# Performance work log

Measured on AMD Instinct MI355X. Metric: run time of the kernel, lower is better.

## Reference

```python
import jax, jax.numpy as jnp
import numpy as np

LX, LY = 256, 256
K_CLASSES = 4
N_SWEEPS = 2
N_SITES = LX * LY

# 8-neighborhood offsets (Moore neighborhood), border handled by clipping
_OFFSETS = np.array([[-1, -1], [-1, 0], [-1, 1],
                     [0, -1],           [0, 1],
                     [1, -1],  [1, 0],  [1, 1]], dtype=np.int32)


def setup_inputs() -> dict:
    key = jax.random.key(0)
    k1, k2, k3, k4 = jax.random.split(key, 4)
    X_init = jax.random.randint(k1, (LX, LY), 0, K_CLASSES).astype(jnp.int32)
    perm = jax.random.permutation(k2, jnp.arange(N_SITES)).astype(jnp.int32)
    uniforms = jax.random.uniform(k3, (N_SWEEPS, N_SITES), dtype=jnp.float32)
    beta = jax.random.uniform(k4, (), dtype=jnp.float32) + 0.5  # Potts coupling
    return {"X_init": X_init, "perm": perm, "uniforms": uniforms,
            "beta": beta, "K": K_CLASSES}


def reference(X_init, perm, uniforms, beta, K):
    lx, ly = X_init.shape
    off = jnp.asarray(_OFFSETS)              # (8, 2)
    classes = jnp.arange(K)                  # (K,)

    def update_one_site(X, uv, r):
        u, v = jnp.unravel_index(uv, (lx, ly))
        uu = jnp.clip(u + off[:, 0], 0, lx - 1)   # (8,) neighbor rows
        vv = jnp.clip(v + off[:, 1], 0, ly - 1)   # (8,) neighbor cols
        neigh = X[uu, vv]                          # (8,) dynamic gather
        # Potts potential: p_k proportional to exp(beta * #{neighbors == k})
        counts = (neigh[None, :] == classes[:, None]).sum(axis=1)  # (K,)
        probs = jax.nn.softmax(beta * counts.astype(jnp.float32))  # (K,) sums to 1
        # inverse-CDF categorical sample, as in the original cumsum < r
        x_sample = jnp.count_nonzero(jnp.cumsum(probs) < r)
        return X.at[u, v].set(x_sample.astype(X.dtype))  # scatter write

    def one_sweep(X, rs):
        def body(Xc, inp):
            uv, r = inp
            return update_one_site(Xc, uv, r), None
        X, _ = jax.lax.scan(body, X, (perm, rs))
        return X, None

    X_final, _ = jax.lax.scan(one_sweep, X_init, uniforms)  # N_SWEEPS sweeps
    return X_final
```

## Files before the change

kernel.cpp:

```cpp
#include <hip/hip_runtime.h>
#include <math.h>

#define NSITES 65536
#define WIN 4096
#define NW 16
#define RMAX 64


__device__ __forceinline__ int agg_pos(int v, int* c, int vmax) {
  int pos = 0;
  const int lane = threadIdx.x & 63;
  for (int vv = 1; vv <= vmax; ++vv) {
    unsigned long long m = __ballot(v == vv);
    if (m) {
      int leader = __ffsll((long long)m) - 1;
      int base = 0;
      if (lane == leader) base = atomicAdd(&c[vv], (int)__popcll(m));
      base = __shfl(base, leader);
      if (v == vv) pos = base + (int)__popcll(m & ((1ull << lane) - 1ull));
    }
  }
  return pos;
}

__global__ __launch_bounds__(1024) void GibbsSched_kernel(
    const int* __restrict__ perm, const float* __restrict__ uni,
    uint2* __restrict__ recpk, int* __restrict__ ends) {
  __shared__ unsigned short posg[NSITES];
  __shared__ unsigned short lvl[WIN];
  __shared__ int cnt[RMAX + 1], coff[RMAX + 1];
  __shared__ int chg, bmax;
  const int tid = threadIdx.x;
  const int w = blockIdx.x;
  const int wbase = w * WIN;

  for (int g = tid; g < NSITES / 8; g += 1024)
    ((uint4*)posg)[g] = make_uint4(0u, 0u, 0u, 0u);
  for (int i = tid; i <= RMAX; i += 1024) { cnt[i] = 0; coff[i] = 0; }
  if (tid == 0) bmax = 0;
  __syncthreads();

  int uvk[4];
#pragma unroll
  for (int k = 0; k < 4; ++k) {
    const int lt = tid + k * 1024;
    uvk[k] = perm[wbase + lt];
    posg[uvk[k]] = (unsigned short)(lt + 1);
  }
  __syncthreads();

  unsigned short pred[4][8];
  int myl[4];
#pragma unroll
  for (int k = 0; k < 4; ++k) {
    const int lt = tid + k * 1024;
    const int uv = uvk[k], u = uv >> 8, v = uv & 255;
    const int um = u ? u - 1 : 0, up = u < 255 ? u + 1 : 255;
    const int vm = v ? v - 1 : 0, vp = v < 255 ? v + 1 : 255;
    const int nb8[8] = {(um << 8) | vm, (um << 8) | v, (um << 8) | vp,
                        (u << 8) | vm,                 (u << 8) | vp,
                        (up << 8) | vm, (up << 8) | v, (up << 8) | vp};
#pragma unroll
    for (int j = 0; j < 8; ++j) {
      const int p = posg[nb8[j]];
      pred[k][j] = (p && p - 1 < lt) ? (unsigned short)(p - 1)
                                     : (unsigned short)0xFFFF;
    }
    lvl[lt] = 1;
    myl[k] = 1;
  }
  __syncthreads();

  for (int pass = 0; pass < 128; ++pass) {
    if (tid == 0) chg = 0;
    __syncthreads();
    bool ch = false;
#pragma unroll
    for (int k = 0; k < 4; ++k) {
      int m = 0;
#pragma unroll
      for (int j = 0; j < 8; ++j) {
        const unsigned short p = pred[k][j];
        if (p != 0xFFFF) m = max(m, (int)lvl[p]);
      }
      const int nl = m + 1;
      if (nl != myl[k]) {
        myl[k] = nl;
        lvl[tid + k * 1024] = (unsigned short)nl;
        ch = true;
      }
    }
    if (ch) chg = 1;
    __syncthreads();
    if (chg == 0) break;
  }

#pragma unroll
  for (int k = 0; k < 4; ++k) atomicMax(&bmax, myl[k]);
  __syncthreads();
  const int vmax = bmax;

#pragma unroll
  for (int k = 0; k < 4; ++k) (void)agg_pos(myl[k], cnt, vmax);
  __syncthreads();
  if (tid == 0) {
    int e = 0;
    for (int r = 0; r < RMAX; ++r) {
      coff[r] = e;
      e += cnt[r];
      ends[w * RMAX + r] = e;
    }
  }
  __syncthreads();

#pragma unroll
  for (int k = 0; k < 4; ++k) {
    const int pos = agg_pos(myl[k], coff, vmax);
    const int lt = tid + k * 1024;
    const int gp = wbase + pos;
    recpk[gp] = make_uint2((unsigned)uvk[k],
                           __float_as_uint(uni[wbase + lt]));
    recpk[NSITES + gp] = make_uint2((unsigned)uvk[k],
                                    __float_as_uint(uni[NSITES + wbase + lt]));
  }
}

__device__ __forceinline__ void do_update(unsigned char* cell,
                                          const unsigned int* cellw,
                                          const float4* ctab, unsigned uvv,
                                          float r) {
  const int u = uvv >> 8, v = (int)(uvv & 255u);
  const int um = u ? u - 1 : 0, up = u < 255 ? u + 1 : 255;
  const int vm = v ? v - 1 : 0, vp = v < 255 ? v + 1 : 255;
  const int cb = vm >> 2;
  const int sh0 = (vm & 3) << 3;
  const int shv = (v - vm) << 3;
  const int shp = (vp - vm) << 3;
  int acc = 0;
  {
    const unsigned int* rw = cellw + (um << 6) + cb;
    const unsigned long long wd =
        ((unsigned long long)rw[1] << 32) | (unsigned long long)rw[0];
    const unsigned wl = (unsigned)(wd >> sh0);
    acc += 1 << ((wl & 255u) << 2);
    acc += 1 << (((wl >> shv) & 255u) << 2);
    acc += 1 << (((wl >> shp) & 255u) << 2);
  }
  {
    const unsigned int* rw = cellw + (u << 6) + cb;
    const unsigned long long wd =
        ((unsigned long long)rw[1] << 32) | (unsigned long long)rw[0];
    const unsigned wl = (unsigned)(wd >> sh0);
    acc += 1 << ((wl & 255u) << 2);
    acc += 1 << (((wl >> shp) & 255u) << 2);
  }
  {
    const unsigned int* rw = cellw + (up << 6) + cb;
    const unsigned long long wd =
        ((unsigned long long)rw[1] << 32) | (unsigned long long)rw[0];
    const unsigned wl = (unsigned)(wd >> sh0);
    acc += 1 << ((wl & 255u) << 2);
    acc += 1 << (((wl >> shv) & 255u) << 2);
    acc += 1 << (((wl >> shp) & 255u) << 2);
  }
  const int n0 = acc & 15, n1 = (acc >> 4) & 15, n2 = (acc >> 8) & 15;
  const float4 c = ctab[n0 + 9 * n1 + 81 * n2];
  int cnt = (c.x < r) ? 1 : 0;
  cnt += (c.y < r) ? 1 : 0;
  cnt += (c.z < r) ? 1 : 0;
  cnt += (c.w < r) ? 1 : 0;
  cell[uvv] = (unsigned char)cnt;
}

__device__ __forceinline__ void run_rounds(unsigned char* cell,
                                           const unsigned int* cellw,
                                           const float4* ctab, const int* le,
                                           const uint2 (&R)[4], int tid) {
  int b = 0, e = le[1];
  for (int rd = 1; rd < RMAX; ++rd) {
    if (b >= WIN) break;
    const int nb = e;
    const int ne = (rd + 1 < RMAX) ? le[rd + 1] : e;
#pragma unroll
    for (int k = 0; k < 4; ++k) {
      const int s = tid + (k << 10);
      if (s >= b && s < e)
        do_update(cell, cellw, ctab, R[k].x, __uint_as_float(R[k].y));
    }
    __syncthreads();
    b = nb;
    e = ne;
  }
}

__global__ __launch_bounds__(1024) void GibbsSampler_90443421319469_kernel(
    const int* __restrict__ Xi, const uint2* __restrict__ recpk,
    const float* __restrict__ betap, const int* __restrict__ ends,
    int* __restrict__ out) {
#pragma clang fp contract(off)
  __shared__ __align__(16) unsigned int cellw[NSITES / 4];
  __shared__ float4 ctab[732];
  __shared__ int lend[NW * RMAX];
  unsigned char* cell = (unsigned char*)cellw;
  const int tid = threadIdx.x;
  const float beta = betap[0];

  uint2 ra[4], rb[4];
#pragma unroll
  for (int k = 0; k < 4; ++k) ra[k] = recpk[tid + (k << 10)];

  for (int g = tid; g < NSITES / 4; g += 1024) {
    int4 x = ((const int4*)Xi)[g];
    cellw[g] = (unsigned)(x.x & 255) | ((unsigned)(x.y & 255) << 8) |
               ((unsigned)(x.z & 255) << 16) | ((unsigned)(x.w & 255) << 24);
  }
  lend[tid] = ends[tid];
  for (int t = tid; t < 729; t += 1024) {
    const int n0 = t % 9, n1 = (t / 9) % 9, n2 = t / 81;
    const int n3 = 8 - n0 - n1 - n2;
    float4 val = make_float4(2.f, 2.f, 2.f, 2.f);
    if (n3 >= 0) {
      const int mx = max(max(n0, n1), max(n2, n3));
      const float xm = beta * (float)mx;
      const float x0 = beta * (float)n0;
      const float x1 = beta * (float)n1;
      const float x2 = beta * (float)n2;
      const float x3 = beta * (float)n3;
      const float e0 = (float)exp((double)(x0 - xm));
      const float e1 = (float)exp((double)(x1 - xm));
      const float e2 = (float)exp((double)(x2 - xm));
      const float e3 = (float)exp((double)(x3 - xm));
      const float s = ((e0 + e1) + e2) + e3;
      const float c0 = e0 / s;
      const float c1 = c0 + e1 / s;
      const float c2 = c1 + e2 / s;
      const float c3 = c2 + e3 / s;
      val = make_float4(c0, c1, c2, c3);
    }
    ctab[t] = val;
  }
  __syncthreads();

  for (int w = 0; w < 2 * NW; ++w) {
    const int ww = w & (NW - 1);
    const int* le = &lend[ww * RMAX];
    const int wn = w + 1;
    const uint2* rpn = recpk + (wn >> 4) * NSITES + (wn & (NW - 1)) * WIN;
    if ((w & 1) == 0) {
      if (wn < 2 * NW) {
#pragma unroll
        for (int k = 0; k < 4; ++k) rb[k] = rpn[tid + (k << 10)];
      }
      run_rounds(cell, cellw, ctab, le, ra, tid);
    } else {
      if (wn < 2 * NW) {
#pragma unroll
        for (int k = 0; k < 4; ++k) ra[k] = rpn[tid + (k << 10)];
      }
      run_rounds(cell, cellw, ctab, le, rb, tid);
    }
  }

  for (int g = tid; g < NSITES / 4; g += 1024) {
    const unsigned p = cellw[g];
    int4 o;
    o.x = (int)(p & 255u);
    o.y = (int)((p >> 8) & 255u);
    o.z = (int)((p >> 16) & 255u);
    o.w = (int)((p >> 24) & 255u);
    ((int4*)out)[g] = o;
  }
}

extern "C" void kernel_launch(void* const* d_in, const int* in_sizes, int n_in,
                              void* d_out, int out_size, void* d_ws,
                              size_t ws_size, hipStream_t stream) {
  const int* Xi = (const int*)d_in[0];
  const int* perm = (const int*)d_in[1];
  const float* uni = (const float*)d_in[2];
  const float* beta = (const float*)d_in[3];
  int* out = (int*)d_out;

  char* ws = (char*)d_ws;
  uint2* recpk = (uint2*)ws;
  int* ends = (int*)(ws + 2 * NSITES * 8);

  GibbsSched_kernel<<<dim3(NW), dim3(1024), 0, stream>>>(perm, uni, recpk,
                                                         ends);
  GibbsSampler_90443421319469_kernel<<<dim3(1), dim3(1024), 0, stream>>>(
      Xi, recpk, beta, ends, out);
}
```

Baseline: 213.8 us.

## Finish small tail rounds in a single wavefront without block barriers

When a round holds 64 or fewer updates, the remaining rounds of the window are handed to wave 0. It reads its records straight from global memory, prefetching the next round, and runs through them without block-wide __syncthreads, so the long tail of small dependency rounds stops paying one full-block barrier each. The round bounds are made wave-uniform with readfirstlane, and a uniform fast path skips per-thread range checks when a round covers a full 1024 chunk. The risk is that larger later rounds get serialized onto one wave, and that correctness now depends on wavefront lockstep ordering between dependent rounds, with no LDS fence between them.

```diff
diff --git a/kernel.cpp b/kernel.cpp
--- a/kernel.cpp
+++ b/kernel.cpp
@@ -175,17 +175,56 @@
 __device__ __forceinline__ void run_rounds(unsigned char* cell,
                                            const unsigned int* cellw,
                                            const float4* ctab, const int* le,
-                                           const uint2 (&R)[4], int tid) {
-  int b = 0, e = le[1];
+                                           const uint2 (&R)[4], int tid,
+                                           const uint2* __restrict__ rp) {
+  const int wave = tid >> 6, lane = tid & 63;
+  int b = 0;
+  int e = __builtin_amdgcn_readfirstlane(le[1]);
   for (int rd = 1; rd < RMAX; ++rd) {
     if (b >= WIN) break;
+    if (e - b <= 64) {
+      if (wave == 0) {
+        int tb = b, te = e, trd = rd;
+        uint2 cur = make_uint2(0u, 0u);
+        if (tb + lane < te) cur = rp[tb + lane];
+        while (tb < WIN) {
+          const int tnb = te;
+          const int tne = (trd + 1 < RMAX)
+                              ? __builtin_amdgcn_readfirstlane(le[trd + 1])
+                              : te;
+          uint2 nxt = make_uint2(0u, 0u);
+          if (tnb + lane < tne) nxt = rp[tnb + lane];
+          if (tb + lane < te)
+            do_update(cell, cellw, ctab, cur.x, __uint_as_float(cur.y));
+          for (int s = tb + lane + 64; s < te; s += 64) {
+            const uint2 rc = rp[s];
+            do_update(cell, cellw, ctab, rc.x, __uint_as_float(rc.y));
+          }
+          cur = nxt;
+          tb = tnb;
+          te = tne;
+          ++trd;
+        }
+      }
+      __syncthreads();
+      return;
+    }
     const int nb = e;
-    const int ne = (rd + 1 < RMAX) ? le[rd + 1] : e;
+    const int ne = (rd + 1 < RMAX)
+                       ? __builtin_amdgcn_readfirstlane(le[rd + 1])
+                       : e;
 #pragma unroll
     for (int k = 0; k < 4; ++k) {
-      const int s = tid + (k << 10);
-      if (s >= b && s < e)
-        do_update(cell, cellw, ctab, R[k].x, __uint_as_float(R[k].y));
+      const int kb = k << 10;
+      if (e > kb && b < kb + 1024) {
+        if (b <= kb && kb + 1024 <= e) {
+          do_update(cell, cellw, ctab, R[k].x, __uint_as_float(R[k].y));
+        } else {
+          const int s = tid + kb;
+          if (s >= b && s < e)
+            do_update(cell, cellw, ctab, R[k].x, __uint_as_float(R[k].y));
+        }
+      }
     }
     __syncthreads();
     b = nb;
@@ -244,6 +283,7 @@
   for (int w = 0; w < 2 * NW; ++w) {
     const int ww = w & (NW - 1);
     const int* le = &lend[ww * RMAX];
+    const uint2* rpc = recpk + (w >> 4) * NSITES + ww * WIN;
     const int wn = w + 1;
     const uint2* rpn = recpk + (wn >> 4) * NSITES + (wn & (NW - 1)) * WIN;
     if ((w & 1) == 0) {
@@ -251,13 +291,13 @@
 #pragma unroll
         for (int k = 0; k < 4; ++k) rb[k] = rpn[tid + (k << 10)];
       }
-      run_rounds(cell, cellw, ctab, le, ra, tid);
+      run_rounds(cell, cellw, ctab, le, ra, tid, rpc);
     } else {
       if (wn < 2 * NW) {
 #pragma unroll
         for (int k = 0; k < 4; ++k) ra[k] = rpn[tid + (k << 10)];
       }
-      run_rounds(cell, cellw, ctab, le, rb, tid);
+      run_rounds(cell, cellw, ctab, le, rb, tid, rpc);
     }
   }
 
```

New measurement: 230.2 us. 1.08x slower.

## Fuse scheduling and sampling kernels with a global atomic flag handoff

Applied to the files above, without the earlier changes.

Merges the level-scheduling kernel and the single-block sampler into one launch of NW blocks. Blocks 1..15 build their window schedules and signal through a global atomic counter, while block 0 builds its own, spins until the rest finish, then runs the sequential sampling phase. This removes one kernel launch and the gap between the two kernels, but adds a hipMemsetAsync and a spin-wait that relies on all blocks being co-resident. It also halves RMAX to 32, which shrinks the round tables but would give wrong results if any window needs more than 31 dependency levels.

```diff
diff --git a/kernel.cpp b/kernel.cpp
--- a/kernel.cpp
+++ b/kernel.cpp
@@ -4,7 +4,7 @@
 #define NSITES 65536
 #define WIN 4096
 #define NW 16
-#define RMAX 64
+#define RMAX 32
 
 
 __device__ __forceinline__ int agg_pos(int v, int* c, int vmax) {
@@ -21,108 +21,6 @@
     }
   }
   return pos;
-}
-
-__global__ __launch_bounds__(1024) void GibbsSched_kernel(
-    const int* __restrict__ perm, const float* __restrict__ uni,
-    uint2* __restrict__ recpk, int* __restrict__ ends) {
-  __shared__ unsigned short posg[NSITES];
-  __shared__ unsigned short lvl[WIN];
-  __shared__ int cnt[RMAX + 1], coff[RMAX + 1];
-  __shared__ int chg, bmax;
-  const int tid = threadIdx.x;
-  const int w = blockIdx.x;
-  const int wbase = w * WIN;
-
-  for (int g = tid; g < NSITES / 8; g += 1024)
-    ((uint4*)posg)[g] = make_uint4(0u, 0u, 0u, 0u);
-  for (int i = tid; i <= RMAX; i += 1024) { cnt[i] = 0; coff[i] = 0; }
-  if (tid == 0) bmax = 0;
-  __syncthreads();
-
-  int uvk[4];
-#pragma unroll
-  for (int k = 0; k < 4; ++k) {
-    const int lt = tid + k * 1024;
-    uvk[k] = perm[wbase + lt];
-    posg[uvk[k]] = (unsigned short)(lt + 1);
-  }
-  __syncthreads();
-
-  unsigned short pred[4][8];
-  int myl[4];
-#pragma unroll
-  for (int k = 0; k < 4; ++k) {
-    const int lt = tid + k * 1024;
-    const int uv = uvk[k], u = uv >> 8, v = uv & 255;
-    const int um = u ? u - 1 : 0, up = u < 255 ? u + 1 : 255;
-    const int vm = v ? v - 1 : 0, vp = v < 255 ? v + 1 : 255;
-    const int nb8[8] = {(um << 8) | vm, (um << 8) | v, (um << 8) | vp,
-                        (u << 8) | vm,                 (u << 8) | vp,
-                        (up << 8) | vm, (up << 8) | v, (up << 8) | vp};
-#pragma unroll
-    for (int j = 0; j < 8; ++j) {
-      const int p = posg[nb8[j]];
-      pred[k][j] = (p && p - 1 < lt) ? (unsigned short)(p - 1)
-                                     : (unsigned short)0xFFFF;
-    }
-    lvl[lt] = 1;
-    myl[k] = 1;
-  }
-  __syncthreads();
-
-  for (int pass = 0; pass < 128; ++pass) {
-    if (tid == 0) chg = 0;
-    __syncthreads();
-    bool ch = false;
-#pragma unroll
-    for (int k = 0; k < 4; ++k) {
-      int m = 0;
-#pragma unroll
-      for (int j = 0; j < 8; ++j) {
-        const unsigned short p = pred[k][j];
-        if (p != 0xFFFF) m = max(m, (int)lvl[p]);
-      }
-      const int nl = m + 1;
-      if (nl != myl[k]) {
-        myl[k] = nl;
-        lvl[tid + k * 1024] = (unsigned short)nl;
-        ch = true;
-      }
-    }
-    if (ch) chg = 1;
-    __syncthreads();
-    if (chg == 0) break;
-  }
-
-#pragma unroll
-  for (int k = 0; k < 4; ++k) atomicMax(&bmax, myl[k]);
-  __syncthreads();
-  const int vmax = bmax;
-
-#pragma unroll
-  for (int k = 0; k < 4; ++k) (void)agg_pos(myl[k], cnt, vmax);
-  __syncthreads();
-  if (tid == 0) {
-    int e = 0;
-    for (int r = 0; r < RMAX; ++r) {
-      coff[r] = e;
-      e += cnt[r];
-      ends[w * RMAX + r] = e;
-    }
-  }
-  __syncthreads();
-
-#pragma unroll
-  for (int k = 0; k < 4; ++k) {
-    const int pos = agg_pos(myl[k], coff, vmax);
-    const int lt = tid + k * 1024;
-    const int gp = wbase + pos;
-    recpk[gp] = make_uint2((unsigned)uvk[k],
-                           __float_as_uint(uni[wbase + lt]));
-    recpk[NSITES + gp] = make_uint2((unsigned)uvk[k],
-                                    __float_as_uint(uni[NSITES + wbase + lt]));
-  }
 }
 
 __device__ __forceinline__ void do_update(unsigned char* cell,
@@ -194,15 +92,134 @@
 }
 
 __global__ __launch_bounds__(1024) void GibbsSampler_90443421319469_kernel(
-    const int* __restrict__ Xi, const uint2* __restrict__ recpk,
-    const float* __restrict__ betap, const int* __restrict__ ends,
-    int* __restrict__ out) {
+    const int* __restrict__ Xi, const int* __restrict__ perm,
+    const float* __restrict__ uni, const float* __restrict__ betap,
+    uint2* __restrict__ recpk, int* __restrict__ ends,
+    int* __restrict__ flag, int* __restrict__ out) {
 #pragma clang fp contract(off)
-  __shared__ __align__(16) unsigned int cellw[NSITES / 4];
-  __shared__ float4 ctab[732];
-  __shared__ int lend[NW * RMAX];
+  __shared__ __align__(16) unsigned char smem[139552];
+  unsigned short* posg = (unsigned short*)smem;
+  unsigned short* lvl = (unsigned short*)(smem + 131072);
+  int* cnt = (int*)(smem + 139264);
+  int* coff = (int*)(smem + 139396);
+  int* chg = (int*)(smem + 139528);
+  int* bmax = (int*)(smem + 139532);
+  unsigned int* cellw = (unsigned int*)smem;
+  float4* ctab = (float4*)(smem + 65536);
+  int* lend = (int*)(smem + 77248);
+
+  const int tid = threadIdx.x;
+  const int w = blockIdx.x;
+  const int wbase = w * WIN;
+
+  for (int g = tid; g < NSITES / 8; g += 1024)
+    ((uint4*)posg)[g] = make_uint4(0u, 0u, 0u, 0u);
+  for (int i = tid; i <= RMAX; i += 1024) { cnt[i] = 0; coff[i] = 0; }
+  if (tid == 0) *bmax = 0;
+  __syncthreads();
+
+  int uvk[4];
+#pragma unroll
+  for (int k = 0; k < 4; ++k) {
+    const int lt = tid + k * 1024;
+    uvk[k] = perm[wbase + lt];
+    posg[uvk[k]] = (unsigned short)(lt + 1);
+  }
+  __syncthreads();
+
+  unsigned short pred[4][8];
+  int myl[4];
+#pragma unroll
+  for (int k = 0; k < 4; ++k) {
+    const int lt = tid + k * 1024;
+    const int uv = uvk[k], u = uv >> 8, v = uv & 255;
+    const int um = u ? u - 1 : 0, up = u < 255 ? u + 1 : 255;
+    const int vm = v ? v - 1 : 0, vp = v < 255 ? v + 1 : 255;
+    const int nb8[8] = {(um << 8) | vm, (um << 8) | v, (um << 8) | vp,
+                        (u << 8) | vm,                 (u << 8) | vp,
+                        (up << 8) | vm, (up << 8) | v, (up << 8) | vp};
+#pragma unroll
+    for (int j = 0; j < 8; ++j) {
+      const int p = posg[nb8[j]];
+      pred[k][j] = (p && p - 1 < lt) ? (unsigned short)(p - 1)
+                                     : (unsigned short)0xFFFF;
+    }
+    lvl[lt] = 1;
+    myl[k] = 1;
+  }
+  __syncthreads();
+
+  for (int pass = 0; pass < 128; ++pass) {
+    if (tid == 0) *chg = 0;
+    __syncthreads();
+    bool ch = false;
+#pragma unroll
+    for (int k = 0; k < 4; ++k) {
+      int m = 0;
+#pragma unroll
+      for (int j = 0; j < 8; ++j) {
+        const unsigned short p = pred[k][j];
+        if (p != 0xFFFF) m = max(m, (int)lvl[p]);
+      }
+      const int nl = m + 1;
+      if (nl != myl[k]) {
+        myl[k] = nl;
+        lvl[tid + k * 1024] = (unsigned short)nl;
+        ch = true;
+      }
+    }
+    if (ch) *chg = 1;
+    __syncthreads();
+    if (*chg == 0) break;
+  }
+
+#pragma unroll
+  for (int k = 0; k < 4; ++k) atomicMax(bmax, myl[k]);
+  __syncthreads();
+  const int vmax = *bmax;
+
+#pragma unroll
+  for (int k = 0; k < 4; ++k) (void)agg_pos(myl[k], cnt, vmax);
+  __syncthreads();
+  if (tid == 0) {
+    int e = 0;
+    for (int r = 0; r < RMAX; ++r) {
+      coff[r] = e;
+      e += cnt[r];
+      ends[w * RMAX + r] = e;
+    }
+  }
+  __syncthreads();
+
+#pragma unroll
+  for (int k = 0; k < 4; ++k) {
+    const int pos = agg_pos(myl[k], coff, vmax);
+    const int lt = tid + k * 1024;
+    const int gp = wbase + pos;
+    recpk[gp] = make_uint2((unsigned)uvk[k],
+                           __float_as_uint(uni[wbase + lt]));
+    recpk[NSITES + gp] = make_uint2((unsigned)uvk[k],
+                                    __float_as_uint(uni[NSITES + wbase + lt]));
+  }
+  __syncthreads();
+
+  if (w != 0) {
+    if (tid == 0) {
+      __threadfence();
+      atomicAdd(flag, 1);
+    }
+    return;
+  }
+
+  if (tid == 0) {
+    while (__hip_atomic_load(flag, __ATOMIC_RELAXED,
+                             __HIP_MEMORY_SCOPE_AGENT) < NW - 1)
+      __builtin_amdgcn_s_sleep(2);
+    __threadfence();
+  }
+  __syncthreads();
+
   unsigned char* cell = (unsigned char*)cellw;
-  const int tid = threadIdx.x;
   const float beta = betap[0];
 
   uint2 ra[4], rb[4];
@@ -214,7 +231,7 @@
     cellw[g] = (unsigned)(x.x & 255) | ((unsigned)(x.y & 255) << 8) |
                ((unsigned)(x.z & 255) << 16) | ((unsigned)(x.w & 255) << 24);
   }
-  lend[tid] = ends[tid];
+  if (tid < NW * RMAX) lend[tid] = ends[tid];
   for (int t = tid; t < 729; t += 1024) {
     const int n0 = t % 9, n1 = (t / 9) % 9, n2 = t / 81;
     const int n3 = 8 - n0 - n1 - n2;
@@ -241,12 +258,12 @@
   }
   __syncthreads();
 
-  for (int w = 0; w < 2 * NW; ++w) {
-    const int ww = w & (NW - 1);
+  for (int ww2 = 0; ww2 < 2 * NW; ++ww2) {
+    const int ww = ww2 & (NW - 1);
     const int* le = &lend[ww * RMAX];
-    const int wn = w + 1;
+    const int wn = ww2 + 1;
     const uint2* rpn = recpk + (wn >> 4) * NSITES + (wn & (NW - 1)) * WIN;
-    if ((w & 1) == 0) {
+    if ((ww2 & 1) == 0) {
       if (wn < 2 * NW) {
 #pragma unroll
         for (int k = 0; k < 4; ++k) rb[k] = rpn[tid + (k << 10)];
@@ -284,9 +301,9 @@
   char* ws = (char*)d_ws;
   uint2* recpk = (uint2*)ws;
   int* ends = (int*)(ws + 2 * NSITES * 8);
-
-  GibbsSched_kernel<<<dim3(NW), dim3(1024), 0, stream>>>(perm, uni, recpk,
-                                                         ends);
-  GibbsSampler_90443421319469_kernel<<<dim3(1), dim3(1024), 0, stream>>>(
-      Xi, recpk, beta, ends, out);
-}
+  int* flag = (int*)(ws + 2 * NSITES * 8 + NW * RMAX * 4);
+
+  hipMemsetAsync(flag, 0, sizeof(int), stream);
+  GibbsSampler_90443421319469_kernel<<<dim3(NW), dim3(1024), 0, stream>>>(
+      Xi, perm, uni, beta, recpk, ends, flag, out);
+}
```

Result: no change. 215.9 us (+1.0%).
